# Performance work log

Measured on AMD Instinct MI355X. Metric: run time of the kernel, lower is better.

Reference implementation:

```python
import jax, jax.numpy as jnp
import numpy as np

EPS = 1e-5
NQ = 4  # n_qubits
DN = ('NCHW', 'OIHW', 'NCHW')


def _bn2d(h, g, b):
    # training-mode batch norm over (N, H, W)
    m = h.mean((0, 2, 3), keepdims=True)
    v = h.var((0, 2, 3), keepdims=True)
    return (h - m) * jax.lax.rsqrt(v + EPS) * g.reshape(1, -1, 1, 1) + b.reshape(1, -1, 1, 1)


def _pool2(h):
    return jax.lax.reduce_window(h, -jnp.inf, jax.lax.max, (1, 1, 2, 2), (1, 1, 2, 2), 'VALID')


def _apply_1q(state, gate, q):
    # state: [B, 2,2,2,2]; gate: [B,2,2] (batched) or [2,2]
    state = jnp.moveaxis(state, 1 + q, -1)
    if gate.ndim == 3:
        state = jnp.einsum('bij,...j->...i', gate, state.reshape(gate.shape[0], -1, 2)).reshape(state.shape) if False else jnp.einsum('bij,b...j->b...i', gate, state)
    else:
        state = jnp.einsum('ij,b...j->b...i', gate, state)
    return jnp.moveaxis(state, -1, 1 + q)


def _apply_cnot(state, c, t):
    state = jnp.moveaxis(state, (1 + c, 1 + t), (-2, -1))
    flipped = jnp.concatenate([state[..., 0:1, :], state[..., 1:2, ::-1]], axis=-2)
    return jnp.moveaxis(flipped, (-2, -1), (1 + c, 1 + t))


def _circuit(encoded, rz_angles):
    # Batched 4-qubit statevector simulation: RY encoding, then per layer
    # a CNOT chain and RZ rotations; returns <Z_i> per qubit.  [B,NQ] -> [B,NQ]
    B = encoded.shape[0]
    state = jnp.zeros((B,) + (2,) * NQ, jnp.complex64)
    state = state.at[:, 0, 0, 0, 0].set(1.0)
    half = encoded.astype(jnp.float32) / 2.0
    c, s = jnp.cos(half), jnp.sin(half)  # [B, NQ]
    for i in range(NQ):
        ry = jnp.stack([jnp.stack([c[:, i], -s[:, i]], -1),
                        jnp.stack([s[:, i], c[:, i]], -1)], -2).astype(jnp.complex64)
        state = _apply_1q(state, ry, i)
    for l in range(rz_angles.shape[0]):
        for i in range(NQ - 1):
            state = _apply_cnot(state, i, i + 1)
        for i in range(NQ):
            phi = rz_angles[l, i].astype(jnp.float32)
            rz = jnp.diag(jnp.exp(1j * jnp.array([-0.5, 0.5], jnp.float32) * phi)).astype(jnp.complex64)
            state = _apply_1q(state, rz, i)
    probs = state.real ** 2 + state.imag ** 2  # [B,2,2,2,2]
    evs = []
    for i in range(NQ):
        axes = tuple(a for a in range(1, NQ + 1) if a != 1 + i)
        pz = probs.sum(axes)  # [B,2]
        evs.append(pz[:, 0] - pz[:, 1])
    return jnp.stack(evs, -1)  # [B, NQ]


def setup_inputs() -> dict:
    key = jax.random.key(0)
    ks = jax.random.split(key, 6)
    B, H, W = 4096, 32, 32
    return {
        'x': jax.random.normal(ks[0], (B, 1, H, W), jnp.float32),
        'conv1_w': jax.random.normal(ks[1], (8, 1, 3, 3), jnp.float32) * 0.1,
        'conv1_b': jnp.zeros((8,), jnp.float32),
        'bn1_g': jnp.ones((8,), jnp.float32),
        'bn1_b': jnp.zeros((8,), jnp.float32),
        'conv2_w': jax.random.normal(ks[2], (16, 8, 3, 3), jnp.float32) * 0.1,
        'conv2_b': jnp.zeros((16,), jnp.float32),
        'bn2_g': jnp.ones((16,), jnp.float32),
        'bn2_b': jnp.zeros((16,), jnp.float32),
        'rz_angles': jax.random.normal(ks[3], (2, 4), jnp.float32),
        'fc_w': jax.random.normal(ks[4], (4, 4), jnp.float32) * 0.5,
        'fc_b': jnp.zeros((4,), jnp.float32),
        'bn3_g': jnp.ones((4,), jnp.float32),
        'bn3_b': jnp.zeros((4,), jnp.float32),
    }


def reference(x, conv1_w, conv1_b, bn1_g, bn1_b, conv2_w, conv2_b, bn2_g, bn2_b,
              rz_angles, fc_w, fc_b, bn3_g, bn3_b):
    h = jax.lax.conv_general_dilated(x, conv1_w, (1, 1), 'SAME', dimension_numbers=DN)
    h = h + conv1_b.reshape(1, -1, 1, 1)
    h = jnp.maximum(_bn2d(h, bn1_g, bn1_b), 0.0)
    h = _pool2(h)
    h = jax.lax.conv_general_dilated(h, conv2_w, (1, 1), 'SAME', dimension_numbers=DN)
    h = h + conv2_b.reshape(1, -1, 1, 1)
    h = jnp.maximum(_bn2d(h, bn2_g, bn2_b), 0.0)
    h = _pool2(h)
    B = x.shape[0]
    encode = h.reshape(B, -1).mean(1, keepdims=True)      # [B,1]
    encoded = jnp.repeat(encode, NQ, axis=1)              # [B,NQ]
    q_out = _circuit(encoded, rz_angles)                  # [B,NQ]
    out = q_out @ fc_w.T + fc_b                           # [B,4]
    m = out.mean(0, keepdims=True)
    v = out.var(0, keepdims=True)
    return (out - m) * jax.lax.rsqrt(v + EPS) * bn3_g + bn3_b
```

## Files before the change

kernel.cpp:

```cpp
#include <hip/hip_runtime.h>
#include <math.h>

#define EPS_F 1e-5f
static constexpr int BATCH = 4096;

__global__ __launch_bounds__(256) void k1(const float* __restrict__ x,
                                          const float* __restrict__ w1,
                                          float* __restrict__ pooled1,
                                          float* __restrict__ p1sum,
                                          float* __restrict__ p1sq) {
    __shared__ float xs[34 * 34];
    __shared__ float w1s[72];
    __shared__ float h1s[8 * 32 * 32];
    __shared__ float rsum[4][8], rsq[4][8];

    const int b = blockIdx.x, t = threadIdx.x;
    for (int j = t; j < 34 * 34; j += 256) xs[j] = 0.f;
    if (t < 72) w1s[t] = w1[t];
    __syncthreads();
    {
        float4 v4 = reinterpret_cast<const float4*>(x + (size_t)b * 1024)[t];
        int e = t * 4, y = e >> 5, xx = e & 31;
        float* d = &xs[(y + 1) * 34 + xx + 1];
        d[0] = v4.x; d[1] = v4.y; d[2] = v4.z; d[3] = v4.w;
    }
    __syncthreads();

    const int col = t & 31, y0 = t >> 5;
    float acc[4][8];
#pragma unroll
    for (int k = 0; k < 4; ++k)
#pragma unroll
        for (int c = 0; c < 8; ++c) acc[k][c] = 0.f;

#pragma unroll
    for (int ky = 0; ky < 3; ++ky)
#pragma unroll
        for (int kx = 0; kx < 3; ++kx) {
            float w[8];
#pragma unroll
            for (int c = 0; c < 8; ++c) w[c] = w1s[c * 9 + ky * 3 + kx];
#pragma unroll
            for (int k = 0; k < 4; ++k) {
                float xv = xs[(y0 + 8 * k + ky) * 34 + col + kx];
#pragma unroll
                for (int c = 0; c < 8; ++c) acc[k][c] = fmaf(w[c], xv, acc[k][c]);
            }
        }

    float s[8], q[8];
#pragma unroll
    for (int c = 0; c < 8; ++c) { s[c] = 0.f; q[c] = 0.f; }
#pragma unroll
    for (int k = 0; k < 4; ++k)
#pragma unroll
        for (int c = 0; c < 8; ++c) { s[c] += acc[k][c]; q[c] += acc[k][c] * acc[k][c]; }
#pragma unroll
    for (int d = 1; d < 64; d <<= 1)
#pragma unroll
        for (int c = 0; c < 8; ++c) {
            s[c] += __shfl_xor(s[c], d, 64);
            q[c] += __shfl_xor(q[c], d, 64);
        }
    const int wid = t >> 6, lane = t & 63;
    if (lane == 0)
#pragma unroll
        for (int c = 0; c < 8; ++c) { rsum[wid][c] = s[c]; rsq[wid][c] = q[c]; }

#pragma unroll
    for (int k = 0; k < 4; ++k)
#pragma unroll
        for (int c = 0; c < 8; ++c) h1s[c * 1024 + (y0 + 8 * k) * 32 + col] = acc[k][c];
    __syncthreads();

    if (t < 8) {
        p1sum[t * BATCH + b] = rsum[0][t] + rsum[1][t] + rsum[2][t] + rsum[3][t];
        p1sq [t * BATCH + b] = rsq [0][t] + rsq [1][t] + rsq [2][t] + rsq [3][t];
    }
#pragma unroll
    for (int i = 0; i < 8; ++i) {
        int o = t + 256 * i;
        int c = o >> 8, rem = o & 255, py = rem >> 4, px = rem & 15;
        const float* hb = &h1s[c * 1024 + (py * 2) * 32 + px * 2];
        float m = fmaxf(fmaxf(hb[0], hb[1]), fmaxf(hb[32], hb[33]));
        pooled1[(size_t)b * 2048 + o] = m;
    }
}

__global__ __launch_bounds__(256) void k_bnfin(const float* __restrict__ psum,
                                               const float* __restrict__ psq,
                                               const float* __restrict__ g,
                                               const float* __restrict__ beta,
                                               float* __restrict__ scale,
                                               float* __restrict__ shift,
                                               float invN) {
    const int ch = blockIdx.x, t = threadIdx.x;
    float s = 0.f, q = 0.f;
    for (int i = t; i < BATCH; i += 256) {
        s += psum[ch * BATCH + i];
        q += psq [ch * BATCH + i];
    }
    __shared__ float rs[256], rq[256];
    rs[t] = s; rq[t] = q;
    __syncthreads();
    for (int d = 128; d > 0; d >>= 1) {
        if (t < d) { rs[t] += rs[t + d]; rq[t] += rq[t + d]; }
        __syncthreads();
    }
    if (t == 0) {
        float mean = rs[0] * invN;
        float var  = rq[0] * invN - mean * mean;
        float sc   = g[ch] * rsqrtf(var + EPS_F);
        scale[ch] = sc;
        shift[ch] = beta[ch] - mean * sc;
    }
}

__global__ __launch_bounds__(256) void k3(const float* __restrict__ pooled1,
                                          const float* __restrict__ w2,
                                          const float* __restrict__ s1,
                                          const float* __restrict__ sh1,
                                          float* __restrict__ pooled2,
                                          float* __restrict__ p2sum,
                                          float* __restrict__ p2sq) {
    __shared__ float a1s[8 * 18 * 20];
    __shared__ float w2s[1152];
    __shared__ float rsum[16], rsq[16];
    const int b = blockIdx.x, t = threadIdx.x;
    for (int j = t; j < 8 * 18 * 20; j += 256) a1s[j] = 0.f;
    for (int j = t; j < 1152; j += 256) w2s[j] = w2[j];
    __syncthreads();
    {
        const int py = t >> 4, px = t & 15;
#pragma unroll
        for (int i = 0; i < 8; ++i) {
            float v = pooled1[(size_t)b * 2048 + 256 * i + t];
            float val = fmaxf(fmaf(v, s1[i], sh1[i]), 0.f);
            a1s[i * 360 + (py + 1) * 20 + (px + 1)] = val;
        }
    }
    __syncthreads();

    const int oc = t >> 4, y = t & 15;
    float acc[16];
#pragma unroll
    for (int i = 0; i < 16; ++i) acc[i] = 0.f;
#pragma unroll
    for (int ic = 0; ic < 8; ++ic)
#pragma unroll
        for (int ky = 0; ky < 3; ++ky) {
            const float* row = &a1s[ic * 360 + (y + ky) * 20];
            float r[20];
#pragma unroll
            for (int j = 0; j < 5; ++j)
                *reinterpret_cast<float4*>(&r[4 * j]) =
                    *reinterpret_cast<const float4*>(&row[4 * j]);
            const float* wp = &w2s[oc * 72 + ic * 9 + ky * 3];
            float w0 = wp[0], w1v = wp[1], w2v = wp[2];
#pragma unroll
            for (int xx = 0; xx < 16; ++xx)
                acc[xx] = fmaf(w0, r[xx], fmaf(w1v, r[xx + 1], fmaf(w2v, r[xx + 2], acc[xx])));
        }

    float s = 0.f, q = 0.f;
#pragma unroll
    for (int xx = 0; xx < 16; ++xx) { s += acc[xx]; q += acc[xx] * acc[xx]; }
#pragma unroll
    for (int d = 1; d < 16; d <<= 1) { s += __shfl_xor(s, d, 64); q += __shfl_xor(q, d, 64); }
    if (y == 0) { rsum[oc] = s; rsq[oc] = q; }

    float m[16];
#pragma unroll
    for (int xx = 0; xx < 16; ++xx) m[xx] = fmaxf(acc[xx], __shfl_xor(acc[xx], 1, 64));
    if ((y & 1) == 0) {
        float o[8];
#pragma unroll
        for (int px = 0; px < 8; ++px) o[px] = fmaxf(m[2 * px], m[2 * px + 1]);
        float4* dst = reinterpret_cast<float4*>(
            &pooled2[(size_t)b * 1024 + oc * 64 + (y >> 1) * 8]);
        dst[0] = make_float4(o[0], o[1], o[2], o[3]);
        dst[1] = make_float4(o[4], o[5], o[6], o[7]);
    }
    __syncthreads();
    if (t < 16) { p2sum[t * BATCH + b] = rsum[t]; p2sq[t * BATCH + b] = rsq[t]; }
}

__global__ __launch_bounds__(256) void k5(const float* __restrict__ pooled2,
                                          const float* __restrict__ s2,
                                          const float* __restrict__ sh2,
                                          const float* __restrict__ fcw,
                                          const float* __restrict__ fcb,
                                          float* __restrict__ outbuf) {
    const int t = threadIdx.x, lane = t & 63;
    const int b = blockIdx.x * 4 + (t >> 6);
    const float* p = pooled2 + (size_t)b * 1024;
    float sum = 0.f;
#pragma unroll
    for (int i = 0; i < 16; ++i) {
        float v = p[i * 64 + lane];
        v = fmaxf(fmaf(v, s2[i], sh2[i]), 0.f);
        sum += v;
    }
#pragma unroll
    for (int d = 1; d < 64; d <<= 1) sum += __shfl_xor(sum, d, 64);
    if (lane < 4) {
        float e = sum * (1.f / 1024.f);
        float z = cosf(e), z2 = z * z;
        int j = lane;
        float o = fcb[j] + z * (fcw[j * 4 + 0] + fcw[j * 4 + 1])
                         + z2 * (fcw[j * 4 + 2] + fcw[j * 4 + 3]);
        outbuf[(size_t)b * 4 + j] = o;
    }
}

__global__ __launch_bounds__(256) void k6(const float* __restrict__ outbuf,
                                          const float* __restrict__ g3,
                                          const float* __restrict__ b3,
                                          float* __restrict__ sc3,
                                          float* __restrict__ sh3) {
    const int t = threadIdx.x, j = t & 3;
    float s = 0.f, q = 0.f;
    for (int i = t >> 2; i < BATCH; i += 64) {
        float v = outbuf[i * 4 + j];
        s += v; q += v * v;
    }
    __shared__ float rs[256], rq[256];
    rs[t] = s; rq[t] = q;
    __syncthreads();
    for (int d = 128; d >= 4; d >>= 1) {
        if (t < d) { rs[t] += rs[t + d]; rq[t] += rq[t + d]; }
        __syncthreads();
    }
    if (t < 4) {
        float mean = rs[t] * (1.f / BATCH);
        float var  = rq[t] * (1.f / BATCH) - mean * mean;
        float sc   = g3[t] * rsqrtf(var + EPS_F);
        sc3[t] = sc;
        sh3[t] = b3[t] - mean * sc;
    }
}

__global__ __launch_bounds__(256) void k7(const float* __restrict__ outbuf,
                                          const float* __restrict__ sc3,
                                          const float* __restrict__ sh3,
                                          float* __restrict__ out) {
    int idx = blockIdx.x * 256 + threadIdx.x;
    if (idx < BATCH * 4) {
        int j = idx & 3;
        out[idx] = fmaf(outbuf[idx], sc3[j], sh3[j]);
    }
}

extern "C" void kernel_launch(void* const* d_in, const int* in_sizes, int n_in,
                              void* d_out, int out_size, void* d_ws, size_t ws_size,
                              hipStream_t stream) {
    const float* x   = (const float*)d_in[0];
    const float* w1  = (const float*)d_in[1];
    const float* g1  = (const float*)d_in[3];
    const float* b1  = (const float*)d_in[4];
    const float* w2  = (const float*)d_in[5];
    const float* g2  = (const float*)d_in[7];
    const float* b2  = (const float*)d_in[8];
    const float* fcw = (const float*)d_in[10];
    const float* fcb = (const float*)d_in[11];
    const float* g3  = (const float*)d_in[12];
    const float* b3  = (const float*)d_in[13];

    float* ws      = (float*)d_ws;
    float* pooled1 = ws;
    float* pooled2 = pooled1 + (size_t)BATCH * 2048;
    float* p1sum   = pooled2 + (size_t)BATCH * 1024;
    float* p1sq    = p1sum + 8 * BATCH;
    float* p2sum   = p1sq  + 8 * BATCH;
    float* p2sq    = p2sum + 16 * BATCH;
    float* s1      = p2sq  + 16 * BATCH;
    float* sh1     = s1 + 8;
    float* s2      = sh1 + 8;
    float* sh2     = s2 + 16;
    float* outbuf  = sh2 + 16;
    float* sc3     = outbuf + BATCH * 4;
    float* sh3     = sc3 + 4;
    float* out     = (float*)d_out;

    k1<<<BATCH, 256, 0, stream>>>(x, w1, pooled1, p1sum, p1sq);
    k_bnfin<<<8, 256, 0, stream>>>(p1sum, p1sq, g1, b1, s1, sh1,
                                   1.f / (float)((size_t)BATCH * 1024));
    k3<<<BATCH, 256, 0, stream>>>(pooled1, w2, s1, sh1, pooled2, p2sum, p2sq);
    k_bnfin<<<16, 256, 0, stream>>>(p2sum, p2sq, g2, b2, s2, sh2,
                                    1.f / (float)((size_t)BATCH * 256));
    k5<<<BATCH / 4, 256, 0, stream>>>(pooled2, s2, sh2, fcw, fcb, outbuf);
    k6<<<1, 256, 0, stream>>>(outbuf, g3, b3, sc3, sh3);
    k7<<<(BATCH * 4 + 255) / 256, 256, 0, stream>>>(outbuf, sc3, sh3, out);
}
```

Baseline: 189.2 us.

## Pool conv1 in registers, register-block conv2 over four channels, fuse final BN kernels

In k1 the 2x2 max-pool is now done with wavefront shuffles, and a compact pooled tile is written to shared memory and stored to global as float4, replacing the full 32x32x8 staging buffer. k3 now processes four images per block with one wave per image. Each thread computes four output channels from a transposed weight layout, so each input row loaded from shared memory is reused across four channels and each weight read is one float4. The last BN stats and apply kernels are merged into one kernel launched 16 times, each block recomputing the stats. This raises register pressure in k3 and adds redundant stats work in the merged kernel.

```diff
diff --git a/kernel.cpp b/kernel.cpp
--- a/kernel.cpp
+++ b/kernel.cpp
@@ -9,9 +9,9 @@
                                           float* __restrict__ pooled1,
                                           float* __restrict__ p1sum,
                                           float* __restrict__ p1sq) {
-    __shared__ float xs[34 * 34];
+    __shared__ __align__(16) float xs[34 * 34];
     __shared__ float w1s[72];
-    __shared__ float h1s[8 * 32 * 32];
+    __shared__ __align__(16) float ps[2048];
     __shared__ float rsum[4][8], rsq[4][8];
 
     const int b = blockIdx.x, t = threadIdx.x;
@@ -70,21 +70,22 @@
 #pragma unroll
     for (int k = 0; k < 4; ++k)
 #pragma unroll
-        for (int c = 0; c < 8; ++c) h1s[c * 1024 + (y0 + 8 * k) * 32 + col] = acc[k][c];
+        for (int c = 0; c < 8; ++c) {
+            float vm = fmaxf(acc[k][c], __shfl_xor(acc[k][c], 32, 64));
+            float hm = fmaxf(vm, __shfl_xor(vm, 1, 64));
+            if ((lane & 33) == 0)
+                ps[c * 256 + (4 * k + wid) * 16 + (col >> 1)] = hm;
+        }
     __syncthreads();
 
     if (t < 8) {
         p1sum[t * BATCH + b] = rsum[0][t] + rsum[1][t] + rsum[2][t] + rsum[3][t];
         p1sq [t * BATCH + b] = rsq [0][t] + rsq [1][t] + rsq [2][t] + rsq [3][t];
     }
-#pragma unroll
-    for (int i = 0; i < 8; ++i) {
-        int o = t + 256 * i;
-        int c = o >> 8, rem = o & 255, py = rem >> 4, px = rem & 15;
-        const float* hb = &h1s[c * 1024 + (py * 2) * 32 + px * 2];
-        float m = fmaxf(fmaxf(hb[0], hb[1]), fmaxf(hb[32], hb[33]));
-        pooled1[(size_t)b * 2048 + o] = m;
-    }
+    float4 o0 = *reinterpret_cast<const float4*>(&ps[t * 8]);
+    float4 o1 = *reinterpret_cast<const float4*>(&ps[t * 8 + 4]);
+    float4* dst = reinterpret_cast<float4*>(&pooled1[(size_t)b * 2048 + t * 8]);
+    dst[0] = o0; dst[1] = o1;
 }
 
 __global__ __launch_bounds__(256) void k_bnfin(const float* __restrict__ psum,
@@ -116,6 +117,30 @@
     }
 }
 
+__device__ __forceinline__ void k3_stats_pool(const float* acc, int oc, int b, int y,
+                                              float* __restrict__ pooled2,
+                                              float* __restrict__ p2sum,
+                                              float* __restrict__ p2sq) {
+    float s = 0.f, q = 0.f;
+#pragma unroll
+    for (int xx = 0; xx < 16; ++xx) { s += acc[xx]; q += acc[xx] * acc[xx]; }
+#pragma unroll
+    for (int d = 1; d < 16; d <<= 1) { s += __shfl_xor(s, d, 64); q += __shfl_xor(q, d, 64); }
+    float vm[16];
+#pragma unroll
+    for (int xx = 0; xx < 16; ++xx) vm[xx] = fmaxf(acc[xx], __shfl_xor(acc[xx], 1, 64));
+    if ((y & 1) == 0) {
+        float4 h0 = make_float4(fmaxf(vm[0], vm[1]),  fmaxf(vm[2], vm[3]),
+                                fmaxf(vm[4], vm[5]),  fmaxf(vm[6], vm[7]));
+        float4 h1 = make_float4(fmaxf(vm[8], vm[9]),  fmaxf(vm[10], vm[11]),
+                                fmaxf(vm[12], vm[13]), fmaxf(vm[14], vm[15]));
+        float4* d2 = reinterpret_cast<float4*>(
+            &pooled2[(size_t)b * 1024 + oc * 64 + (y >> 1) * 8]);
+        d2[0] = h0; d2[1] = h1;
+    }
+    if (y == 0) { p2sum[oc * BATCH + b] = s; p2sq[oc * BATCH + b] = q; }
+}
+
 __global__ __launch_bounds__(256) void k3(const float* __restrict__ pooled1,
                                           const float* __restrict__ w2,
                                           const float* __restrict__ s1,
@@ -123,66 +148,75 @@
                                           float* __restrict__ pooled2,
                                           float* __restrict__ p2sum,
                                           float* __restrict__ p2sq) {
-    __shared__ float a1s[8 * 18 * 20];
-    __shared__ float w2s[1152];
-    __shared__ float rsum[16], rsq[16];
-    const int b = blockIdx.x, t = threadIdx.x;
-    for (int j = t; j < 8 * 18 * 20; j += 256) a1s[j] = 0.f;
-    for (int j = t; j < 1152; j += 256) w2s[j] = w2[j];
-    __syncthreads();
+    __shared__ __align__(16) float a1s[4][2880];
+    __shared__ __align__(16) float w2t[1152];
+    const int t = threadIdx.x;
+    const int e = t >> 6, lane = t & 63;
+    const int o = lane >> 4, y = lane & 15;
+    const int b = blockIdx.x * 4 + e;
+
     {
-        const int py = t >> 4, px = t & 15;
-#pragma unroll
-        for (int i = 0; i < 8; ++i) {
-            float v = pooled1[(size_t)b * 2048 + 256 * i + t];
-            float val = fmaxf(fmaf(v, s1[i], sh1[i]), 0.f);
-            a1s[i * 360 + (py + 1) * 20 + (px + 1)] = val;
-        }
-    }
-    __syncthreads();
-
-    const int oc = t >> 4, y = t & 15;
-    float acc[16];
-#pragma unroll
-    for (int i = 0; i < 16; ++i) acc[i] = 0.f;
+        float4 z = make_float4(0.f, 0.f, 0.f, 0.f);
+        float* base = &a1s[0][0];
+        for (int j = t; j < 2880; j += 256)
+            *reinterpret_cast<float4*>(&base[j * 4]) = z;
+    }
+    for (int j = t; j < 1152; j += 256) {
+        int oc = j / 72, r = j - oc * 72;
+        w2t[r * 16 + oc] = w2[j];
+    }
+    __syncthreads();
+
+    float s1r[8], sh1r[8];
+#pragma unroll
+    for (int c = 0; c < 8; ++c) { s1r[c] = s1[c]; sh1r[c] = sh1[c]; }
+
+    {
+        const float* src = pooled1 + (size_t)b * 2048;
+        float* dst = &a1s[e][0];
+#pragma unroll
+        for (int i = 0; i < 32; ++i) {
+            int idx = i * 64 + lane;
+            int c = idx >> 8, rem = idx & 255, py = rem >> 4, px = rem & 15;
+            float v = fmaxf(fmaf(src[idx], s1r[c], sh1r[c]), 0.f);
+            dst[c * 360 + (py + 1) * 20 + (px + 1)] = v;
+        }
+    }
+    __syncthreads();
+
+    float acc0[16], acc1[16], acc2[16], acc3[16];
+#pragma unroll
+    for (int i = 0; i < 16; ++i) { acc0[i] = 0.f; acc1[i] = 0.f; acc2[i] = 0.f; acc3[i] = 0.f; }
+
 #pragma unroll
     for (int ic = 0; ic < 8; ++ic)
 #pragma unroll
         for (int ky = 0; ky < 3; ++ky) {
-            const float* row = &a1s[ic * 360 + (y + ky) * 20];
+            const float* row = &a1s[e][ic * 360 + (y + ky) * 20];
             float r[20];
 #pragma unroll
             for (int j = 0; j < 5; ++j)
                 *reinterpret_cast<float4*>(&r[4 * j]) =
                     *reinterpret_cast<const float4*>(&row[4 * j]);
-            const float* wp = &w2s[oc * 72 + ic * 9 + ky * 3];
-            float w0 = wp[0], w1v = wp[1], w2v = wp[2];
-#pragma unroll
-            for (int xx = 0; xx < 16; ++xx)
-                acc[xx] = fmaf(w0, r[xx], fmaf(w1v, r[xx + 1], fmaf(w2v, r[xx + 2], acc[xx])));
-        }
-
-    float s = 0.f, q = 0.f;
-#pragma unroll
-    for (int xx = 0; xx < 16; ++xx) { s += acc[xx]; q += acc[xx] * acc[xx]; }
-#pragma unroll
-    for (int d = 1; d < 16; d <<= 1) { s += __shfl_xor(s, d, 64); q += __shfl_xor(q, d, 64); }
-    if (y == 0) { rsum[oc] = s; rsq[oc] = q; }
-
-    float m[16];
-#pragma unroll
-    for (int xx = 0; xx < 16; ++xx) m[xx] = fmaxf(acc[xx], __shfl_xor(acc[xx], 1, 64));
-    if ((y & 1) == 0) {
-        float o[8];
-#pragma unroll
-        for (int px = 0; px < 8; ++px) o[px] = fmaxf(m[2 * px], m[2 * px + 1]);
-        float4* dst = reinterpret_cast<float4*>(
-            &pooled2[(size_t)b * 1024 + oc * 64 + (y >> 1) * 8]);
-        dst[0] = make_float4(o[0], o[1], o[2], o[3]);
-        dst[1] = make_float4(o[4], o[5], o[6], o[7]);
-    }
-    __syncthreads();
-    if (t < 16) { p2sum[t * BATCH + b] = rsum[t]; p2sq[t * BATCH + b] = rsq[t]; }
+#pragma unroll
+            for (int kx = 0; kx < 3; ++kx) {
+                float4 w4 = *reinterpret_cast<const float4*>(
+                    &w2t[(ic * 9 + ky * 3 + kx) * 16 + o * 4]);
+#pragma unroll
+                for (int xx = 0; xx < 16; ++xx) {
+                    float rv = r[xx + kx];
+                    acc0[xx] = fmaf(w4.x, rv, acc0[xx]);
+                    acc1[xx] = fmaf(w4.y, rv, acc1[xx]);
+                    acc2[xx] = fmaf(w4.z, rv, acc2[xx]);
+                    acc3[xx] = fmaf(w4.w, rv, acc3[xx]);
+                }
+            }
+        }
+
+    k3_stats_pool(acc0, o * 4 + 0, b, y, pooled2, p2sum, p2sq);
+    k3_stats_pool(acc1, o * 4 + 1, b, y, pooled2, p2sum, p2sq);
+    k3_stats_pool(acc2, o * 4 + 2, b, y, pooled2, p2sum, p2sq);
+    k3_stats_pool(acc3, o * 4 + 3, b, y, pooled2, p2sum, p2sq);
 }
 
 __global__ __launch_bounds__(256) void k5(const float* __restrict__ pooled2,
@@ -213,11 +247,10 @@
     }
 }
 
-__global__ __launch_bounds__(256) void k6(const float* __restrict__ outbuf,
-                                          const float* __restrict__ g3,
-                                          const float* __restrict__ b3,
-                                          float* __restrict__ sc3,
-                                          float* __restrict__ sh3) {
+__global__ __launch_bounds__(256) void k67(const float* __restrict__ outbuf,
+                                           const float* __restrict__ g3,
+                                           const float* __restrict__ b3,
+                                           float* __restrict__ out) {
     const int t = threadIdx.x, j = t & 3;
     float s = 0.f, q = 0.f;
     for (int i = t >> 2; i < BATCH; i += 64) {
@@ -225,6 +258,7 @@
         s += v; q += v * v;
     }
     __shared__ float rs[256], rq[256];
+    __shared__ float sc[4], sh[4];
     rs[t] = s; rq[t] = q;
     __syncthreads();
     for (int d = 128; d >= 4; d >>= 1) {
@@ -234,21 +268,19 @@
     if (t < 4) {
         float mean = rs[t] * (1.f / BATCH);
         float var  = rq[t] * (1.f / BATCH) - mean * mean;
-        float sc   = g3[t] * rsqrtf(var + EPS_F);
-        sc3[t] = sc;
-        sh3[t] = b3[t] - mean * sc;
-    }
-}
-
-__global__ __launch_bounds__(256) void k7(const float* __restrict__ outbuf,
-                                          const float* __restrict__ sc3,
-                                          const float* __restrict__ sh3,
-                                          float* __restrict__ out) {
-    int idx = blockIdx.x * 256 + threadIdx.x;
-    if (idx < BATCH * 4) {
-        int j = idx & 3;
-        out[idx] = fmaf(outbuf[idx], sc3[j], sh3[j]);
-    }
+        float s3   = g3[t] * rsqrtf(var + EPS_F);
+        sc[t] = s3;
+        sh[t] = b3[t] - mean * s3;
+    }
+    __syncthreads();
+    int base = blockIdx.x * 1024 + t * 4;
+    float4 v = *reinterpret_cast<const float4*>(&outbuf[base]);
+    float4 r;
+    r.x = fmaf(v.x, sc[0], sh[0]);
+    r.y = fmaf(v.y, sc[1], sh[1]);
+    r.z = fmaf(v.z, sc[2], sh[2]);
+    r.w = fmaf(v.w, sc[3], sh[3]);
+    *reinterpret_cast<float4*>(&out[base]) = r;
 }
 
 extern "C" void kernel_launch(void* const* d_in, const int* in_sizes, int n_in,
@@ -278,17 +310,14 @@
     float* s2      = sh1 + 8;
     float* sh2     = s2 + 16;
     float* outbuf  = sh2 + 16;
-    float* sc3     = outbuf + BATCH * 4;
-    float* sh3     = sc3 + 4;
     float* out     = (float*)d_out;
 
     k1<<<BATCH, 256, 0, stream>>>(x, w1, pooled1, p1sum, p1sq);
     k_bnfin<<<8, 256, 0, stream>>>(p1sum, p1sq, g1, b1, s1, sh1,
                                    1.f / (float)((size_t)BATCH * 1024));
-    k3<<<BATCH, 256, 0, stream>>>(pooled1, w2, s1, sh1, pooled2, p2sum, p2sq);
+    k3<<<BATCH / 4, 256, 0, stream>>>(pooled1, w2, s1, sh1, pooled2, p2sum, p2sq);
     k_bnfin<<<16, 256, 0, stream>>>(p2sum, p2sq, g2, b2, s2, sh2,
                                     1.f / (float)((size_t)BATCH * 256));
     k5<<<BATCH / 4, 256, 0, stream>>>(pooled2, s2, sh2, fcw, fcb, outbuf);
-    k6<<<1, 256, 0, stream>>>(outbuf, g3, b3, sc3, sh3);
-    k7<<<(BATCH * 4 + 255) / 256, 256, 0, stream>>>(outbuf, sc3, sh3, out);
-}
+    k67<<<16, 256, 0, stream>>>(outbuf, g3, b3, out);
+}
```

New measurement: 394.5 us. 2.09x slower.
